# Kernel tuning notes

Measured on AMD Instinct MI355X. Metric: run time of the kernel, lower is better.

Reference implementation:

```python
import jax, jax.numpy as jnp
import numpy as np


def setup_inputs() -> dict:
    key = jax.random.key(0)
    k1, k2 = jax.random.split(key)
    N = 50000
    E = 800000
    out_features = 64
    edge = jax.random.randint(k1, (2, E), 0, N, dtype=jnp.int64)
    edge_w = jax.random.normal(k2, (E, out_features), dtype=jnp.float32)
    return {"edge": edge, "edge_w": edge_w, "N": N, "E": E, "out_features": out_features}


def reference(edge, edge_w, N, E, out_features):
    # sparse_coo_tensor(edge, edge_w, [N, N, F]) summed over dim=1 reduces to a
    # segment-sum of edge values over the row (source) index edge[0].
    # output[i, f] = sum_{e: edge[0,e]==i} edge_w[e, f]   -> [N, out_features]
    return jax.ops.segment_sum(edge_w, edge[0], num_segments=N)
```

## Files before the change

### kernel.cpp

```cpp
#include <hip/hip_runtime.h>


#define CEDGE 4096
#define WROWS 256
#define SHIFT 8
#define STCAP 8192

__global__ __launch_bounds__(256) void bucket_hist(
    const int* __restrict__ edge0, int* __restrict__ cnt,
    int E, int nblk, int NB)
{
    __shared__ int lh[256];
    int t = threadIdx.x, blk = blockIdx.x;
    lh[t] = 0;
    __syncthreads();
    #pragma unroll
    for (int j = 0; j < 4; ++j) {
        int idx4 = blk * 1024 + j * 256 + t;
        int base = idx4 * 4;
        if (base + 3 < E) {
            int4 r = ((const int4*)edge0)[idx4];
            atomicAdd(&lh[r.x >> SHIFT], 1);
            atomicAdd(&lh[r.y >> SHIFT], 1);
            atomicAdd(&lh[r.z >> SHIFT], 1);
            atomicAdd(&lh[r.w >> SHIFT], 1);
        } else {
            for (int i = base; i < E && i < base + 4; ++i)
                atomicAdd(&lh[edge0[i] >> SHIFT], 1);
        }
    }
    __syncthreads();
    if (t < NB) cnt[t * nblk + blk] = lh[t];
}

__global__ __launch_bounds__(1024) void scan_flat(int* __restrict__ a, int M)
{
    __shared__ int wsums[16];
    __shared__ int carryS;
    int t = threadIdx.x, lane = t & 63, wv = t >> 6;
    if (t == 0) carryS = 0;
    __syncthreads();
    for (int base = 0; base < M; base += 1024) {
        int i = base + t;
        int v = (i < M) ? a[i] : 0;
        int inc = v;
        #pragma unroll
        for (int off = 1; off < 64; off <<= 1) {
            int u = __shfl_up(inc, off);
            if (lane >= off) inc += u;
        }
        if (lane == 63) wsums[wv] = inc;
        __syncthreads();
        int wpre = 0;
        for (int w = 0; w < wv; ++w) wpre += wsums[w];
        int c = carryS;
        if (i < M) a[i] = c + wpre + inc - v;
        __syncthreads();
        if (t == 1023) carryS = c + wpre + inc;
    }
}

__global__ __launch_bounds__(256) void bucket_scatter(
    const int* __restrict__ edge0, const int* __restrict__ cntS,
    int* __restrict__ recs , int E, int nblk, int NB)
{
    __shared__ int lh[256];
    __shared__ int so[256];
    __shared__ int gb[256];
    __shared__ int ws4[4];
    __shared__ int2 stage[CEDGE];
    int t = threadIdx.x, lane = t & 63, wv = t >> 6, blk = blockIdx.x;
    lh[t] = 0;
    if (t < NB) gb[t] = cntS[t * nblk + blk];
    __syncthreads();

    int rowR[16], rkR[16];
    #pragma unroll
    for (int j = 0; j < 4; ++j) {
        int idx4 = blk * 1024 + j * 256 + t;
        int base = idx4 * 4;
        if (base + 3 < E) {
            int4 r = ((const int4*)edge0)[idx4];
            rowR[j*4+0] = r.x; rkR[j*4+0] = atomicAdd(&lh[r.x >> SHIFT], 1);
            rowR[j*4+1] = r.y; rkR[j*4+1] = atomicAdd(&lh[r.y >> SHIFT], 1);
            rowR[j*4+2] = r.z; rkR[j*4+2] = atomicAdd(&lh[r.z >> SHIFT], 1);
            rowR[j*4+3] = r.w; rkR[j*4+3] = atomicAdd(&lh[r.w >> SHIFT], 1);
        } else {
            #pragma unroll
            for (int c = 0; c < 4; ++c) {
                int i = base + c;
                if (i < E) {
                    int rr = edge0[i];
                    rowR[j*4+c] = rr;
                    rkR[j*4+c]  = atomicAdd(&lh[rr >> SHIFT], 1);
                } else {
                    rowR[j*4+c] = -1;
                    rkR[j*4+c]  = 0;
                }
            }
        }
    }
    __syncthreads();
    {
        int v = lh[t];
        int inc = v;
        #pragma unroll
        for (int off = 1; off < 64; off <<= 1) {
            int u = __shfl_up(inc, off);
            if (lane >= off) inc += u;
        }
        if (lane == 63) ws4[wv] = inc;
        __syncthreads();
        int wpre = 0;
        for (int w = 0; w < wv; ++w) wpre += ws4[w];
        so[t] = wpre + inc - v;
    }
    __syncthreads();
    #pragma unroll
    for (int k = 0; k < 16; ++k) {
        int row = rowR[k];
        if (row >= 0) {
            int b = row >> SHIFT;
            int id = blk * CEDGE + ((k >> 2) * 256 + t) * 4 + (k & 3);
            stage[so[b] + rkR[k]] = make_int2(row, id);
        }
    }
    __syncthreads();
    int Ctot = E - blk * CEDGE; if (Ctot > CEDGE) Ctot = CEDGE;
    int2* rout = (int2*)recs;
    for (int p = t; p < Ctot; p += 256) {
        int2 rec = stage[p];
        int b = rec.x >> SHIFT;
        rout[gb[b] + (p - so[b])] = rec;
    }
}

__global__ __launch_bounds__(1024) void bucket_csr(
    const int* __restrict__ cntS, const int* __restrict__ recs,
    int* __restrict__ offsets, int* __restrict__ ids,
    int E, int nblk, int NB, int N)
{
    __shared__ int rowCnt[WROWS];
    __shared__ int rowFill[WROWS];
    __shared__ int rowPre[WROWS];
    __shared__ int ws4[4];
    __shared__ int stage[STCAP];
    int t = threadIdx.x, b = blockIdx.x;
    int lane = t & 63, wv = t >> 6;
    int S0 = cntS[b * nblk];
    int S1 = (b + 1 < NB) ? cntS[(b + 1) * nblk] : E;
    int cnt = S1 - S0;
    if (t < WROWS) { rowCnt[t] = 0; rowFill[t] = 0; }
    __syncthreads();
    const int2* rin = (const int2*)recs;
    for (int k = t; k < cnt; k += 1024) {
        int2 r = rin[S0 + k];
        atomicAdd(&rowCnt[r.x - (b << SHIFT)], 1);
    }
    __syncthreads();
    int v = (t < WROWS) ? rowCnt[t] : 0;
    int inc = v;
    #pragma unroll
    for (int off = 1; off < 64; off <<= 1) {
        int u = __shfl_up(inc, off);
        if (lane >= off) inc += u;
    }
    if (lane == 63 && wv < 4) ws4[wv] = inc;
    __syncthreads();
    if (t < WROWS) {
        int wpre = 0;
        for (int w = 0; w < wv; ++w) wpre += ws4[w];
        int ex = wpre + inc - v;
        rowPre[t] = ex;
        int gr = (b << SHIFT) + t;
        if (gr < N) offsets[gr] = S0 + ex;
    }
    if (b == NB - 1 && t == 0) offsets[N] = E;
    __syncthreads();
    bool inLds = (cnt <= STCAP);
    for (int k = t; k < cnt; k += 1024) {
        int2 r = rin[S0 + k];
        int lr = r.x - (b << SHIFT);
        int pos = rowPre[lr] + atomicAdd(&rowFill[lr], 1);
        if (inLds) stage[pos] = r.y;
        else       ids[S0 + pos] = r.y;
    }
    __syncthreads();
    if (inLds)
        for (int k = t; k < cnt; k += 1024) ids[S0 + k] = stage[k];
}

__global__ __launch_bounds__(256) void reduce_kernel(
    const int* __restrict__ offsets, const int* __restrict__ ids,
    const float4* __restrict__ w4, float4* __restrict__ out4, int N)
{
    int row = blockIdx.x * 4 + (threadIdx.x >> 6);
    if (row >= N) return;
    int lane = threadIdx.x & 63;
    int sub = lane >> 3, g = lane & 7;
    int beg = offsets[row], end = offsets[row + 1];
    int deg = end - beg;

    float4 a0 = make_float4(0.f, 0.f, 0.f, 0.f);
    float4 a1 = make_float4(0.f, 0.f, 0.f, 0.f);

    int nloc = deg < 64 ? deg : 64;
    int myid = (lane < deg) ? ids[beg + lane] : 0;

    const float4* __restrict__ wp = w4 + g * 2;

    int full = nloc & ~15;
    for (int b = 0; b < full; b += 16) {
        int e0 = __shfl(myid, b + sub);
        int e1 = __shfl(myid, b + 8 + sub);
        float4 w00 = wp[(size_t)e0 * 16];
        float4 w01 = wp[(size_t)e0 * 16 + 1];
        float4 w10 = wp[(size_t)e1 * 16];
        float4 w11 = wp[(size_t)e1 * 16 + 1];
        a0.x += w00.x + w10.x; a0.y += w00.y + w10.y;
        a0.z += w00.z + w10.z; a0.w += w00.w + w10.w;
        a1.x += w01.x + w11.x; a1.y += w01.y + w11.y;
        a1.z += w01.z + w11.z; a1.w += w01.w + w11.w;
    }
    if (full < nloc) {
        int s0 = full + sub;
        int s1 = full + 8 + sub;
        int e0 = __shfl(myid, s0 & 63);
        int e1 = __shfl(myid, s1 & 63);
        if (s0 < nloc) {
            float4 w0 = wp[(size_t)e0 * 16];
            float4 w1 = wp[(size_t)e0 * 16 + 1];
            a0.x += w0.x; a0.y += w0.y; a0.z += w0.z; a0.w += w0.w;
            a1.x += w1.x; a1.y += w1.y; a1.z += w1.z; a1.w += w1.w;
        }
        if (s1 < nloc) {
            float4 w0 = wp[(size_t)e1 * 16];
            float4 w1 = wp[(size_t)e1 * 16 + 1];
            a0.x += w0.x; a0.y += w0.y; a0.z += w0.z; a0.w += w0.w;
            a1.x += w1.x; a1.y += w1.y; a1.z += w1.z; a1.w += w1.w;
        }
    }
    for (int j = beg + 64 + sub; j < end; j += 8) {
        int e = ids[j];
        float4 w0 = wp[(size_t)e * 16];
        float4 w1 = wp[(size_t)e * 16 + 1];
        a0.x += w0.x; a0.y += w0.y; a0.z += w0.z; a0.w += w0.w;
        a1.x += w1.x; a1.y += w1.y; a1.z += w1.z; a1.w += w1.w;
    }

    #pragma unroll
    for (int m = 8; m < 64; m <<= 1) {
        a0.x += __shfl_xor(a0.x, m); a0.y += __shfl_xor(a0.y, m);
        a0.z += __shfl_xor(a0.z, m); a0.w += __shfl_xor(a0.w, m);
        a1.x += __shfl_xor(a1.x, m); a1.y += __shfl_xor(a1.y, m);
        a1.z += __shfl_xor(a1.z, m); a1.w += __shfl_xor(a1.w, m);
    }
    if (sub == 0) {
        out4[(size_t)row * 16 + g * 2]     = a0;
        out4[(size_t)row * 16 + g * 2 + 1] = a1;
    }
}

extern "C" void kernel_launch(void* const* d_in, const int* in_sizes, int n_in,
                              void* d_out, int out_size, void* d_ws, size_t ws_size,
                              hipStream_t stream) {
    const int*   edge   = (const int*)d_in[0];
    const float* edge_w = (const float*)d_in[1];
    int E = in_sizes[0] / 2;
    int N = out_size / 64;
    int nblk = (E + CEDGE - 1) / CEDGE;
    int NB   = (N + WROWS - 1) / WROWS;

    int* recs    = (int*)d_ws;
    int* cntS    = recs + 2 * (size_t)E;
    int* offsets = cntS + (size_t)NB * nblk;
    int* ids     = offsets + N + 1;

    bucket_hist   <<<nblk, 256, 0, stream>>>(edge, cntS, E, nblk, NB);
    scan_flat     <<<1, 1024, 0, stream>>>(cntS, NB * nblk);
    bucket_scatter<<<nblk, 256, 0, stream>>>(edge, cntS, recs, E, nblk, NB);
    bucket_csr    <<<NB, 1024, 0, stream>>>(cntS, recs, offsets, ids, E, nblk, NB, N);

    int blocksR = (N + 3) / 4;
    reduce_kernel <<<blocksR, 256, 0, stream>>>(offsets, ids, (const float4*)edge_w,
                                                (float4*)d_out, N);
}
```

Baseline: 354.5 us.

## Parallelize bucket-count scan and fuse CSR build with reduction via LDS atomics

Replaces the single-block serial scan with a two-pass multi-block scan (tile sums, then per-tile exclusive scan). It also removes the per-row CSR construction and the separate gather-reduce kernel. Each bucket block now reads its bucket's (row,id) records directly and accumulates the 64-wide rows into a 128x64 shared-memory float accumulator with LDS atomics, in two halves. This drops the offsets/ids passes and a launch, but each block scans its records twice. Only 196 blocks run the gather, and LDS float atomics may contend on hot rows.

```diff
diff --git a/kernel.cpp b/kernel.cpp
--- a/kernel.cpp
+++ b/kernel.cpp
@@ -4,7 +4,7 @@
 #define CEDGE 4096
 #define WROWS 256
 #define SHIFT 8
-#define STCAP 8192
+#define TILE 1024
 
 __global__ __launch_bounds__(256) void bucket_hist(
     const int* __restrict__ edge0, int* __restrict__ cnt,
@@ -33,35 +33,73 @@
     if (t < NB) cnt[t * nblk + blk] = lh[t];
 }
 
-__global__ __launch_bounds__(1024) void scan_flat(int* __restrict__ a, int M)
-{
-    __shared__ int wsums[16];
-    __shared__ int carryS;
-    int t = threadIdx.x, lane = t & 63, wv = t >> 6;
-    if (t == 0) carryS = 0;
-    __syncthreads();
-    for (int base = 0; base < M; base += 1024) {
-        int i = base + t;
-        int v = (i < M) ? a[i] : 0;
-        int inc = v;
+__global__ __launch_bounds__(256) void scan_partial(
+    const int* __restrict__ a, int* __restrict__ tileSum, int M)
+{
+    __shared__ int wsum[4];
+    int t = threadIdx.x;
+    int base = blockIdx.x * TILE + t * 4;
+    int s = 0;
+    #pragma unroll
+    for (int k = 0; k < 4; ++k) {
+        int i = base + k;
+        if (i < M) s += a[i];
+    }
+    for (int off = 1; off < 64; off <<= 1) s += __shfl_xor(s, off);
+    if ((t & 63) == 0) wsum[t >> 6] = s;
+    __syncthreads();
+    if (t == 0) tileSum[blockIdx.x] = wsum[0] + wsum[1] + wsum[2] + wsum[3];
+}
+
+__global__ __launch_bounds__(256) void scan_final(
+    const int* __restrict__ a, const int* __restrict__ tileSum,
+    int* __restrict__ ax, int M, int numTiles)
+{
+    __shared__ int wtot[4];
+    __shared__ int tilePre;
+    int t = threadIdx.x;
+    int lane = t & 63, wv = t >> 6;
+
+    if (t < 64) {
+        int v0 = (t < numTiles) ? tileSum[t] : 0;
+        int v = v0;
         #pragma unroll
         for (int off = 1; off < 64; off <<= 1) {
-            int u = __shfl_up(inc, off);
-            if (lane >= off) inc += u;
-        }
-        if (lane == 63) wsums[wv] = inc;
-        __syncthreads();
-        int wpre = 0;
-        for (int w = 0; w < wv; ++w) wpre += wsums[w];
-        int c = carryS;
-        if (i < M) a[i] = c + wpre + inc - v;
-        __syncthreads();
-        if (t == 1023) carryS = c + wpre + inc;
+            int u = __shfl_up(v, off);
+            if (t >= off) v += u;
+        }
+        if (t == blockIdx.x) tilePre = v - v0;
+    }
+
+    int base = blockIdx.x * TILE + t * 4;
+    int c[4]; int s = 0;
+    #pragma unroll
+    for (int k = 0; k < 4; ++k) {
+        int i = base + k;
+        c[k] = (i < M) ? a[i] : 0;
+        s += c[k];
+    }
+    int inc = s;
+    #pragma unroll
+    for (int off = 1; off < 64; off <<= 1) {
+        int u = __shfl_up(inc, off);
+        if (lane >= off) inc += u;
+    }
+    if (lane == 63) wtot[wv] = inc;
+    __syncthreads();
+    int wpre = 0;
+    for (int w = 0; w < wv; ++w) wpre += wtot[w];
+    int pre = tilePre + wpre + (inc - s);
+    #pragma unroll
+    for (int k = 0; k < 4; ++k) {
+        int i = base + k;
+        if (i < M) ax[i] = pre;
+        pre += c[k];
     }
 }
 
 __global__ __launch_bounds__(256) void bucket_scatter(
-    const int* __restrict__ edge0, const int* __restrict__ cntS,
+    const int* __restrict__ edge0, const int* __restrict__ cntX,
     int* __restrict__ recs , int E, int nblk, int NB)
 {
     __shared__ int lh[256];
@@ -71,7 +109,7 @@
     __shared__ int2 stage[CEDGE];
     int t = threadIdx.x, lane = t & 63, wv = t >> 6, blk = blockIdx.x;
     lh[t] = 0;
-    if (t < NB) gb[t] = cntS[t * nblk + blk];
+    if (t < NB) gb[t] = cntX[t * nblk + blk];
     __syncthreads();
 
     int rowR[16], rkR[16];
@@ -135,129 +173,44 @@
     }
 }
 
-__global__ __launch_bounds__(1024) void bucket_csr(
-    const int* __restrict__ cntS, const int* __restrict__ recs,
-    int* __restrict__ offsets, int* __restrict__ ids,
+__global__ __launch_bounds__(1024) void bucket_reduce(
+    const int* __restrict__ cntX, const int* __restrict__ recs,
+    const float* __restrict__ w, float* __restrict__ out,
     int E, int nblk, int NB, int N)
 {
-    __shared__ int rowCnt[WROWS];
-    __shared__ int rowFill[WROWS];
-    __shared__ int rowPre[WROWS];
-    __shared__ int ws4[4];
-    __shared__ int stage[STCAP];
-    int t = threadIdx.x, b = blockIdx.x;
-    int lane = t & 63, wv = t >> 6;
-    int S0 = cntS[b * nblk];
-    int S1 = (b + 1 < NB) ? cntS[(b + 1) * nblk] : E;
-    int cnt = S1 - S0;
-    if (t < WROWS) { rowCnt[t] = 0; rowFill[t] = 0; }
-    __syncthreads();
+    __shared__ float acc[128][64];
+    int t = threadIdx.x, lane = t & 63, wv = t >> 6;
+    int b = blockIdx.x;
+    int S0 = cntX[b * nblk];
+    int S1 = (b + 1 < NB) ? cntX[(b + 1) * nblk] : E;
     const int2* rin = (const int2*)recs;
-    for (int k = t; k < cnt; k += 1024) {
-        int2 r = rin[S0 + k];
-        atomicAdd(&rowCnt[r.x - (b << SHIFT)], 1);
-    }
-    __syncthreads();
-    int v = (t < WROWS) ? rowCnt[t] : 0;
-    int inc = v;
-    #pragma unroll
-    for (int off = 1; off < 64; off <<= 1) {
-        int u = __shfl_up(inc, off);
-        if (lane >= off) inc += u;
-    }
-    if (lane == 63 && wv < 4) ws4[wv] = inc;
-    __syncthreads();
-    if (t < WROWS) {
-        int wpre = 0;
-        for (int w = 0; w < wv; ++w) wpre += ws4[w];
-        int ex = wpre + inc - v;
-        rowPre[t] = ex;
-        int gr = (b << SHIFT) + t;
-        if (gr < N) offsets[gr] = S0 + ex;
-    }
-    if (b == NB - 1 && t == 0) offsets[N] = E;
-    __syncthreads();
-    bool inLds = (cnt <= STCAP);
-    for (int k = t; k < cnt; k += 1024) {
-        int2 r = rin[S0 + k];
-        int lr = r.x - (b << SHIFT);
-        int pos = rowPre[lr] + atomicAdd(&rowFill[lr], 1);
-        if (inLds) stage[pos] = r.y;
-        else       ids[S0 + pos] = r.y;
-    }
-    __syncthreads();
-    if (inLds)
-        for (int k = t; k < cnt; k += 1024) ids[S0 + k] = stage[k];
-}
-
-__global__ __launch_bounds__(256) void reduce_kernel(
-    const int* __restrict__ offsets, const int* __restrict__ ids,
-    const float4* __restrict__ w4, float4* __restrict__ out4, int N)
-{
-    int row = blockIdx.x * 4 + (threadIdx.x >> 6);
-    if (row >= N) return;
-    int lane = threadIdx.x & 63;
-    int sub = lane >> 3, g = lane & 7;
-    int beg = offsets[row], end = offsets[row + 1];
-    int deg = end - beg;
-
-    float4 a0 = make_float4(0.f, 0.f, 0.f, 0.f);
-    float4 a1 = make_float4(0.f, 0.f, 0.f, 0.f);
-
-    int nloc = deg < 64 ? deg : 64;
-    int myid = (lane < deg) ? ids[beg + lane] : 0;
-
-    const float4* __restrict__ wp = w4 + g * 2;
-
-    int full = nloc & ~15;
-    for (int b = 0; b < full; b += 16) {
-        int e0 = __shfl(myid, b + sub);
-        int e1 = __shfl(myid, b + 8 + sub);
-        float4 w00 = wp[(size_t)e0 * 16];
-        float4 w01 = wp[(size_t)e0 * 16 + 1];
-        float4 w10 = wp[(size_t)e1 * 16];
-        float4 w11 = wp[(size_t)e1 * 16 + 1];
-        a0.x += w00.x + w10.x; a0.y += w00.y + w10.y;
-        a0.z += w00.z + w10.z; a0.w += w00.w + w10.w;
-        a1.x += w01.x + w11.x; a1.y += w01.y + w11.y;
-        a1.z += w01.z + w11.z; a1.w += w01.w + w11.w;
-    }
-    if (full < nloc) {
-        int s0 = full + sub;
-        int s1 = full + 8 + sub;
-        int e0 = __shfl(myid, s0 & 63);
-        int e1 = __shfl(myid, s1 & 63);
-        if (s0 < nloc) {
-            float4 w0 = wp[(size_t)e0 * 16];
-            float4 w1 = wp[(size_t)e0 * 16 + 1];
-            a0.x += w0.x; a0.y += w0.y; a0.z += w0.z; a0.w += w0.w;
-            a1.x += w1.x; a1.y += w1.y; a1.z += w1.z; a1.w += w1.w;
-        }
-        if (s1 < nloc) {
-            float4 w0 = wp[(size_t)e1 * 16];
-            float4 w1 = wp[(size_t)e1 * 16 + 1];
-            a0.x += w0.x; a0.y += w0.y; a0.z += w0.z; a0.w += w0.w;
-            a1.x += w1.x; a1.y += w1.y; a1.z += w1.z; a1.w += w1.w;
-        }
-    }
-    for (int j = beg + 64 + sub; j < end; j += 8) {
-        int e = ids[j];
-        float4 w0 = wp[(size_t)e * 16];
-        float4 w1 = wp[(size_t)e * 16 + 1];
-        a0.x += w0.x; a0.y += w0.y; a0.z += w0.z; a0.w += w0.w;
-        a1.x += w1.x; a1.y += w1.y; a1.z += w1.z; a1.w += w1.w;
-    }
-
-    #pragma unroll
-    for (int m = 8; m < 64; m <<= 1) {
-        a0.x += __shfl_xor(a0.x, m); a0.y += __shfl_xor(a0.y, m);
-        a0.z += __shfl_xor(a0.z, m); a0.w += __shfl_xor(a0.w, m);
-        a1.x += __shfl_xor(a1.x, m); a1.y += __shfl_xor(a1.y, m);
-        a1.z += __shfl_xor(a1.z, m); a1.w += __shfl_xor(a1.w, m);
-    }
-    if (sub == 0) {
-        out4[(size_t)row * 16 + g * 2]     = a0;
-        out4[(size_t)row * 16 + g * 2 + 1] = a1;
+
+    for (int half = 0; half < 2; ++half) {
+        #pragma unroll
+        for (int k = 0; k < 8; ++k) ((float*)acc)[k * 1024 + t] = 0.f;
+        __syncthreads();
+
+        for (int base = S0 + wv * 64; base < S1; base += 16 * 64) {
+            int m = S1 - base; if (m > 64) m = 64;
+            int2 my = (lane < m) ? rin[base + lane] : make_int2(-1, 0);
+            for (int j = 0; j < m; ++j) {
+                int row = __shfl(my.x, j);
+                int lr  = row & (WROWS - 1);
+                if ((lr >> 7) == half) {
+                    int id = __shfl(my.y, j);
+                    float v = w[(size_t)id * 64 + lane];
+                    atomicAdd(&acc[lr & 127][lane], v);
+                }
+            }
+        }
+        __syncthreads();
+
+        int r0 = (b << SHIFT) + (half << 7);
+        for (int rr = wv; rr < 128; rr += 16) {
+            int gr = r0 + rr;
+            if (gr < N) out[(size_t)gr * 64 + lane] = acc[rr][lane];
+        }
+        __syncthreads();
     }
 }
 
@@ -270,18 +223,18 @@
     int N = out_size / 64;
     int nblk = (E + CEDGE - 1) / CEDGE;
     int NB   = (N + WROWS - 1) / WROWS;
+    int M    = NB * nblk;
+    int numTiles = (M + TILE - 1) / TILE;
 
     int* recs    = (int*)d_ws;
     int* cntS    = recs + 2 * (size_t)E;
-    int* offsets = cntS + (size_t)NB * nblk;
-    int* ids     = offsets + N + 1;
+    int* cntX    = cntS + M;
+    int* tileSum = cntX + M;
 
     bucket_hist   <<<nblk, 256, 0, stream>>>(edge, cntS, E, nblk, NB);
-    scan_flat     <<<1, 1024, 0, stream>>>(cntS, NB * nblk);
-    bucket_scatter<<<nblk, 256, 0, stream>>>(edge, cntS, recs, E, nblk, NB);
-    bucket_csr    <<<NB, 1024, 0, stream>>>(cntS, recs, offsets, ids, E, nblk, NB, N);
-
-    int blocksR = (N + 3) / 4;
-    reduce_kernel <<<blocksR, 256, 0, stream>>>(offsets, ids, (const float4*)edge_w,
-                                                (float4*)d_out, N);
-}
+    scan_partial  <<<numTiles, 256, 0, stream>>>(cntS, tileSum, M);
+    scan_final    <<<numTiles, 256, 0, stream>>>(cntS, tileSum, cntX, M, numTiles);
+    bucket_scatter<<<nblk, 256, 0, stream>>>(edge, cntX, recs, E, nblk, NB);
+    bucket_reduce <<<NB, 1024, 0, stream>>>(cntX, recs, edge_w, (float*)d_out,
+                                            E, nblk, NB, N);
+}
```

Result: slower. 684.9 us (+93.2%).
